# Performance work log

Hardware: AMD Instinct MI355X
Metric: run time of the kernel (lower is better)

The kernel has to match this reference:

```python
import jax, jax.numpy as jnp
import numpy as np

K = 2          # top-k experts kept (init kwarg k)
TEMP = 1.0     # gating temperature


def setup_inputs() -> dict:
    key = jax.random.key(0)
    ks = jax.random.split(key, 5)
    B, S, D, O, E = 4, 2048, 1024, 1024, 8
    scale = 1.0 / np.sqrt(D)
    x = jax.random.normal(ks[0], (B, S, D), dtype=jnp.float32)
    W = jax.random.normal(ks[1], (E, O, D), dtype=jnp.float32) * scale   # per-expert Linear weight [out,in]
    b = jax.random.normal(ks[2], (E, O), dtype=jnp.float32) * 0.01
    Wg = jax.random.normal(ks[3], (E, D), dtype=jnp.float32) * scale     # gate Linear weight [E,in]
    bg = jnp.zeros((E,), dtype=jnp.float32)
    return {"x": x, "W": W, "b": b, "Wg": Wg, "bg": bg}


def reference(x, W, b, Wg, bg):
    # gating: softmax over experts (per token, segment_expert_trigger=False)
    gate_logits = (jnp.einsum('bsd,ed->bse', x, Wg) + bg) / TEMP
    gate_scores = jax.nn.softmax(gate_logits, axis=-1)                   # [B,S,E]
    topk_scores, topk_idx = jax.lax.top_k(gate_scores, K)                # [B,S,K]
    # dense all-expert projection (matches torch.stack of per-expert Linear)
    expert_outputs = jnp.einsum('bsd,eod->bseo', x, W) + b               # [B,S,E,O]
    # gather the top-k expert outputs, scale by gate score, and sum
    selected = jnp.take_along_axis(expert_outputs, topk_idx[..., None], axis=2)  # [B,S,K,O]
    output = jnp.sum(selected * topk_scores[..., None], axis=2)          # [B,S,O]
    return output
```

## Files before the change

### kernel.cpp

```cpp
#include <hip/hip_runtime.h>
#include <hip/hip_bf16.h>

#define NTOK 8192
#define DDIM 1024
#define ODIM 1024
#define NEXP 8
#define BK   64
#define NKT  (DDIM / BK)

typedef __attribute__((ext_vector_type(8))) short short8;
typedef __attribute__((ext_vector_type(4))) float f32x4;

#define CNT_OFF   0u
#define SC_OFF    256u
#define LIST_OFF  (128u * 1024u)
#define XH_OFF    (1u<<20)
#define WH_OFF    ((1u<<20) + NTOK*DDIM*2u)

__device__ inline unsigned short f2bf(float f) {
    unsigned int u = __float_as_uint(f);
    unsigned int r = (u + 0x7FFFu + ((u >> 16) & 1u)) >> 16;
    return (unsigned short)r;
}

__device__ inline void glds16(const unsigned short* g, unsigned short* l) {
    __builtin_amdgcn_global_load_lds(
        (const __attribute__((address_space(1))) unsigned int*)g,
        (__attribute__((address_space(3))) unsigned int*)l, 16, 0, 0);
}

__global__ void k_zero(int* counts) {
    if (threadIdx.x < 16) counts[threadIdx.x] = 0;
}

__global__ void k_cvt(const float4* __restrict__ src, ushort4* __restrict__ dst, int n4) {
    int i = blockIdx.x * blockDim.x + threadIdx.x;
    if (i >= n4) return;
    float4 v = src[i];
    ushort4 o;
    o.x = f2bf(v.x); o.y = f2bf(v.y); o.z = f2bf(v.z); o.w = f2bf(v.w);
    dst[i] = o;
}

__global__ __launch_bounds__(256) void k_gate(
    const float* __restrict__ x, const float* __restrict__ Wg,
    const float* __restrict__ bg, const float* __restrict__ b,
    float* __restrict__ out, float* __restrict__ scores2,
    int* __restrict__ lists, int* __restrict__ counts,
    unsigned short* __restrict__ xh)
{
    __shared__ unsigned char s_eid[64];
    const int tid = threadIdx.x, wave = tid >> 6, lane = tid & 63;
    const int tblk = blockIdx.x * 32;

    double bgv[NEXP];
    #pragma unroll
    for (int e = 0; e < NEXP; e++) bgv[e] = (double)bg[e];

    for (int ti = 0; ti < 8; ti++) {
        const int t = tblk + wave * 8 + ti;
        const float* xr = x + (size_t)t * DDIM;
        float4 xv[4];
        #pragma unroll
        for (int i = 0; i < 4; i++)
            xv[i] = *(const float4*)&xr[lane * 4 + 256 * i];

        unsigned short* xhr = xh + (size_t)t * DDIM;
        #pragma unroll
        for (int i = 0; i < 4; i++) {
            ushort4 h;
            h.x = f2bf(xv[i].x); h.y = f2bf(xv[i].y);
            h.z = f2bf(xv[i].z); h.w = f2bf(xv[i].w);
            *(ushort4*)&xhr[lane * 4 + 256 * i] = h;
        }

        double lg[NEXP];
        #pragma unroll
        for (int e = 0; e < NEXP; e++) {
            const float* wr = Wg + (size_t)e * DDIM;
            double a = 0.0;
            #pragma unroll
            for (int i = 0; i < 4; i++) {
                float4 wv = *(const float4*)&wr[lane * 4 + 256 * i];
                a += (double)xv[i].x * (double)wv.x + (double)xv[i].y * (double)wv.y
                   + (double)xv[i].z * (double)wv.z + (double)xv[i].w * (double)wv.w;
            }
            #pragma unroll
            for (int off = 32; off > 0; off >>= 1) a += __shfl_xor(a, off);
            lg[e] = a + bgv[e];
        }

        int i0 = -1, i1 = -1;
        double best = -1e300, sec = -1e300;
        #pragma unroll
        for (int e = 0; e < NEXP; e++) {
            double v = lg[e];
            if (v > best) { sec = best; i1 = i0; best = v; i0 = e; }
            else if (v > sec) { sec = v; i1 = e; }
        }
        double sum = 0.0;
        #pragma unroll
        for (int e = 0; e < NEXP; e++) sum += exp(lg[e] - best);
        float s0 = (float)(1.0 / sum);
        float s1 = (float)(exp(sec - best) / sum);

        if (lane == 0) {
            scores2[t * 2 + 0] = s0;
            scores2[t * 2 + 1] = s1;
            int le = (wave * 8 + ti) * 2;
            s_eid[le + 0] = (unsigned char)i0;
            s_eid[le + 1] = (unsigned char)i1;
        }

        const float* b0 = b + (size_t)i0 * ODIM;
        const float* b1 = b + (size_t)i1 * ODIM;
        float* orow = out + (size_t)t * ODIM;
        #pragma unroll
        for (int i = 0; i < 4; i++) {
            int o = lane * 4 + 256 * i;
            float4 v0 = *(const float4*)&b0[o];
            float4 v1 = *(const float4*)&b1[o];
            float4 r;
            r.x = s0 * v0.x + s1 * v1.x;
            r.y = s0 * v0.y + s1 * v1.y;
            r.z = s0 * v0.z + s1 * v1.z;
            r.w = s0 * v0.w + s1 * v1.w;
            *(float4*)&orow[o] = r;
        }
    }
    __syncthreads();

    if (tid < 16) {
        int e = tid & 7, kk = tid >> 3;
        int c = 0;
        for (int j = kk; j < 64; j += 2) c += (s_eid[j] == e);
        if (c) {
            int p = atomicAdd(&counts[tid], c);
            for (int j = kk; j < 64; j += 2)
                if (s_eid[j] == e)
                    lists[tid * NTOK + (p++)] = (tblk + (j >> 1)) * 2 + kk;
        }
    }
}

__global__ __launch_bounds__(256, 2) void k_gemm(
    const unsigned short* __restrict__ xh, const unsigned short* __restrict__ wh,
    const int* __restrict__ counts, const int* __restrict__ lists,
    const float* __restrict__ scores2, float* __restrict__ out)
{
    __shared__ __align__(16) unsigned short As[2][128 * BK];
    __shared__ __align__(16) unsigned short Bs[2][128 * BK];

    const int nwg = (int)gridDim.x;
    int bid = ((int)blockIdx.x & 7) * (nwg >> 3) + ((int)blockIdx.x >> 3);

    int e = -1, mt = 0, nt = 0, cnt = 0;
    #pragma unroll
    for (int ee = 0; ee < NEXP; ee++) {
        int c = counts[ee];
        int tiles = ((c + 127) >> 7) * 8;
        if (e < 0) {
            if (bid < tiles) { e = ee; mt = bid >> 3; nt = bid & 7; cnt = c; }
            else bid -= tiles;
        }
    }
    if (e < 0) return;

    const int m0 = mt * 128, n0 = nt * 128;
    const int* list = lists + e * NTOK;
    const int tid = threadIdx.x, wid = tid >> 6, lane = tid & 63;

    const int l8 = lane >> 3, s8 = lane & 7;
    const int co = ((s8 ^ l8) << 3);
    const unsigned short* whE = wh + (size_t)e * ODIM * DDIM;
    const unsigned short* aSrc[4];
    const unsigned short* bSrc[4];
    int rbase[4];
    #pragma unroll
    for (int i = 0; i < 4; i++) {
        int rb = (wid * 4 + i) * 8;
        rbase[i] = rb;
        int r = rb + l8;
        int g = m0 + r; if (g >= cnt) g = cnt - 1;
        aSrc[i] = xh + (size_t)(list[g] >> 1) * DDIM + co;
        bSrc[i] = whE + (size_t)(n0 + r) * DDIM + co;
    }

    const int wm = wid >> 1, wn = wid & 1;
    const int fr = lane & 15, g4 = lane >> 4;
    const int fx0 = ((g4 ^ (fr & 7)) << 3);
    const int fx1 = (((4 + g4) ^ (fr & 7)) << 3);

    f32x4 acc[4][4];
    #pragma unroll
    for (int m = 0; m < 4; m++)
        #pragma unroll
        for (int n = 0; n < 4; n++)
            acc[m][n] = (f32x4){0.f, 0.f, 0.f, 0.f};

    #pragma unroll
    for (int i = 0; i < 4; i++) {
        glds16(aSrc[i], &As[0][rbase[i] * BK]);
        glds16(bSrc[i], &Bs[0][rbase[i] * BK]);
    }

    int buf = 0;
    for (int t = 0; t < NKT; t++) {
        __syncthreads();
        if (t + 1 < NKT) {
            const int k0 = (t + 1) * BK;
            #pragma unroll
            for (int i = 0; i < 4; i++) {
                glds16(aSrc[i] + k0, &As[buf ^ 1][rbase[i] * BK]);
                glds16(bSrc[i] + k0, &Bs[buf ^ 1][rbase[i] * BK]);
            }
        }
        short8 af[4][2], bfr[4][2];
        #pragma unroll
        for (int m = 0; m < 4; m++) {
            const int row = (wm * 64 + m * 16 + fr) * BK;
            af[m][0] = *(const short8*)&As[buf][row + fx0];
            af[m][1] = *(const short8*)&As[buf][row + fx1];
        }
        #pragma unroll
        for (int n = 0; n < 4; n++) {
            const int row = (wn * 64 + n * 16 + fr) * BK;
            bfr[n][0] = *(const short8*)&Bs[buf][row + fx0];
            bfr[n][1] = *(const short8*)&Bs[buf][row + fx1];
        }
        #pragma unroll
        for (int kk = 0; kk < 2; kk++)
            #pragma unroll
            for (int m = 0; m < 4; m++)
                #pragma unroll
                for (int n = 0; n < 4; n++)
                    acc[m][n] = __builtin_amdgcn_mfma_f32_16x16x32_bf16(
                        af[m][kk], bfr[n][kk], acc[m][n], 0, 0, 0);
        buf ^= 1;
    }

    #pragma unroll
    for (int m = 0; m < 4; m++) {
        #pragma unroll
        for (int j = 0; j < 4; j++) {
            int r = wm * 64 + m * 16 + g4 * 4 + j;
            int gr = m0 + r;
            if (gr < cnt) {
                int entry = list[gr];
                int tok = entry >> 1;
                float s = scores2[entry];
                float* orow = out + (size_t)tok * ODIM + n0 + wn * 64 + fr;
                #pragma unroll
                for (int n = 0; n < 4; n++)
                    orow[n * 16] += s * acc[m][n][j];
            }
        }
    }
}

extern "C" void kernel_launch(void* const* d_in, const int* in_sizes, int n_in,
                              void* d_out, int out_size, void* d_ws, size_t ws_size,
                              hipStream_t stream) {
    const float* x  = (const float*)d_in[0];
    const float* W  = (const float*)d_in[1];
    const float* b  = (const float*)d_in[2];
    const float* Wg = (const float*)d_in[3];
    const float* bg = (const float*)d_in[4];
    float* out = (float*)d_out;
    char* ws = (char*)d_ws;

    int*   counts  = (int*)(ws + CNT_OFF);
    float* scores2 = (float*)(ws + SC_OFF);
    int*   lists   = (int*)(ws + LIST_OFF);
    unsigned short* xh = (unsigned short*)(ws + XH_OFF);
    unsigned short* wh = (unsigned short*)(ws + WH_OFF);

    k_zero<<<1, 64, 0, stream>>>(counts);

    int n4w = NEXP * ODIM * DDIM / 4;
    k_cvt<<<n4w / 256, 256, 0, stream>>>((const float4*)W, (ushort4*)wh, n4w);

    k_gate<<<NTOK / 32, 256, 0, stream>>>(x, Wg, bg, b, out, scores2, lists, counts, xh);

    k_gemm<<<576, 256, 0, stream>>>(xh, wh, counts,     lists,            scores2, out);
    k_gemm<<<576, 256, 0, stream>>>(xh, wh, counts + 8, lists + 8 * NTOK, scores2, out);
}
```

Before: 167.5 us.

## Merge expert GEMMs into one persistent launch with side buffer and smaller tiles

The two per-slot GEMM launches become one persistent, grid-strided kernel that covers all 16 expert lists. Second-slot results go to a separate buffer, and a final add kernel merges it into the output. The change also halves BK to 32 with a new LDS swizzle, raises occupancy to 4 blocks per SM, shrinks the gate kernel to 8 tokens per block with float softmax, and folds the counter zeroing into the weight-convert kernel. The aim is to cut launch count, fill the machine better and avoid serialising the two GEMM passes, at the cost of an extra output-sized buffer plus a read-modify-write pass.

```diff
diff --git a/kernel.cpp b/kernel.cpp
--- a/kernel.cpp
+++ b/kernel.cpp
@@ -5,17 +5,19 @@
 #define DDIM 1024
 #define ODIM 1024
 #define NEXP 8
-#define BK   64
+#define BK   32
 #define NKT  (DDIM / BK)
 
 typedef __attribute__((ext_vector_type(8))) short short8;
 typedef __attribute__((ext_vector_type(4))) float f32x4;
 
 #define CNT_OFF   0u
-#define SC_OFF    256u
+#define SC_OFF    (4u * 1024u)
 #define LIST_OFF  (128u * 1024u)
-#define XH_OFF    (1u<<20)
-#define WH_OFF    ((1u<<20) + NTOK*DDIM*2u)
+#define XH_OFF    (1u << 20)
+#define WH_OFF    ((1u << 20) + 16u*1024u*1024u)
+#define O2_OFF    ((1u << 20) + 32u*1024u*1024u)
+#define WS_NEED   ((size_t)O2_OFF + (size_t)NTOK * ODIM * 4u)
 
 __device__ inline unsigned short f2bf(float f) {
     unsigned int u = __float_as_uint(f);
@@ -29,11 +31,9 @@
         (__attribute__((address_space(3))) unsigned int*)l, 16, 0, 0);
 }
 
-__global__ void k_zero(int* counts) {
-    if (threadIdx.x < 16) counts[threadIdx.x] = 0;
-}
-
-__global__ void k_cvt(const float4* __restrict__ src, ushort4* __restrict__ dst, int n4) {
+__global__ void k_cvtw(const float4* __restrict__ src, ushort4* __restrict__ dst,
+                       int n4, int* __restrict__ counts) {
+    if (blockIdx.x == 0 && threadIdx.x < 16) counts[threadIdx.x] = 0;
     int i = blockIdx.x * blockDim.x + threadIdx.x;
     if (i >= n4) return;
     float4 v = src[i];
@@ -42,23 +42,20 @@
     dst[i] = o;
 }
 
-__global__ __launch_bounds__(256) void k_gate(
+__global__ __launch_bounds__(256, 2) void k_gate(
     const float* __restrict__ x, const float* __restrict__ Wg,
     const float* __restrict__ bg, const float* __restrict__ b,
     float* __restrict__ out, float* __restrict__ scores2,
     int* __restrict__ lists, int* __restrict__ counts,
     unsigned short* __restrict__ xh)
 {
-    __shared__ unsigned char s_eid[64];
+    __shared__ unsigned char s_eid[16];
     const int tid = threadIdx.x, wave = tid >> 6, lane = tid & 63;
-    const int tblk = blockIdx.x * 32;
-
-    double bgv[NEXP];
-    #pragma unroll
-    for (int e = 0; e < NEXP; e++) bgv[e] = (double)bg[e];
-
-    for (int ti = 0; ti < 8; ti++) {
-        const int t = tblk + wave * 8 + ti;
+    const int tblk = blockIdx.x * 8;
+
+    #pragma unroll 1
+    for (int ti = 0; ti < 2; ti++) {
+        const int t = tblk + wave * 2 + ti;
         const float* xr = x + (size_t)t * DDIM;
         float4 xv[4];
         #pragma unroll
@@ -87,7 +84,7 @@
             }
             #pragma unroll
             for (int off = 32; off > 0; off >>= 1) a += __shfl_xor(a, off);
-            lg[e] = a + bgv[e];
+            lg[e] = a + (double)bg[e];
         }
 
         int i0 = -1, i1 = -1;
@@ -98,16 +95,16 @@
             if (v > best) { sec = best; i1 = i0; best = v; i0 = e; }
             else if (v > sec) { sec = v; i1 = e; }
         }
-        double sum = 0.0;
-        #pragma unroll
-        for (int e = 0; e < NEXP; e++) sum += exp(lg[e] - best);
-        float s0 = (float)(1.0 / sum);
-        float s1 = (float)(exp(sec - best) / sum);
+        float sum = 0.f;
+        #pragma unroll
+        for (int e = 0; e < NEXP; e++) sum += expf((float)(lg[e] - best));
+        float s0 = 1.f / sum;
+        float s1 = expf((float)(sec - best)) / sum;
 
         if (lane == 0) {
             scores2[t * 2 + 0] = s0;
             scores2[t * 2 + 1] = s1;
-            int le = (wave * 8 + ti) * 2;
+            int le = (wave * 2 + ti) * 2;
             s_eid[le + 0] = (unsigned char)i0;
             s_eid[le + 1] = (unsigned char)i1;
         }
@@ -133,128 +130,153 @@
     if (tid < 16) {
         int e = tid & 7, kk = tid >> 3;
         int c = 0;
-        for (int j = kk; j < 64; j += 2) c += (s_eid[j] == e);
+        #pragma unroll
+        for (int j = 0; j < 8; j++) c += (s_eid[j * 2 + kk] == e);
         if (c) {
             int p = atomicAdd(&counts[tid], c);
-            for (int j = kk; j < 64; j += 2)
-                if (s_eid[j] == e)
-                    lists[tid * NTOK + (p++)] = (tblk + (j >> 1)) * 2 + kk;
-        }
-    }
-}
-
-__global__ __launch_bounds__(256, 2) void k_gemm(
+            #pragma unroll
+            for (int j = 0; j < 8; j++)
+                if (s_eid[j * 2 + kk] == e)
+                    lists[tid * NTOK + (p++)] = (tblk + j) * 2 + kk;
+        }
+    }
+}
+
+__global__ __launch_bounds__(256, 4) void k_gemm(
     const unsigned short* __restrict__ xh, const unsigned short* __restrict__ wh,
     const int* __restrict__ counts, const int* __restrict__ lists,
-    const float* __restrict__ scores2, float* __restrict__ out)
+    const float* __restrict__ scores2, float* __restrict__ out,
+    float* __restrict__ out2, int listLo, int listHi)
 {
     __shared__ __align__(16) unsigned short As[2][128 * BK];
     __shared__ __align__(16) unsigned short Bs[2][128 * BK];
 
     const int nwg = (int)gridDim.x;
-    int bid = ((int)blockIdx.x & 7) * (nwg >> 3) + ((int)blockIdx.x >> 3);
-
-    int e = -1, mt = 0, nt = 0, cnt = 0;
+    const int bid0 = ((int)blockIdx.x & 7) * (nwg >> 3) + ((int)blockIdx.x >> 3);
+    const int tid = threadIdx.x, wid = tid >> 6, lane = tid & 63;
+
+    int cnts[16];
     #pragma unroll
-    for (int ee = 0; ee < NEXP; ee++) {
-        int c = counts[ee];
-        int tiles = ((c + 127) >> 7) * 8;
-        if (e < 0) {
-            if (bid < tiles) { e = ee; mt = bid >> 3; nt = bid & 7; cnt = c; }
-            else bid -= tiles;
-        }
-    }
-    if (e < 0) return;
-
-    const int m0 = mt * 128, n0 = nt * 128;
-    const int* list = lists + e * NTOK;
-    const int tid = threadIdx.x, wid = tid >> 6, lane = tid & 63;
-
-    const int l8 = lane >> 3, s8 = lane & 7;
-    const int co = ((s8 ^ l8) << 3);
-    const unsigned short* whE = wh + (size_t)e * ODIM * DDIM;
-    const unsigned short* aSrc[4];
-    const unsigned short* bSrc[4];
-    int rbase[4];
+    for (int i = 0; i < 16; i++) cnts[i] = counts[i];
+    int tbLo = 0, tbHi = 0;
     #pragma unroll
-    for (int i = 0; i < 4; i++) {
-        int rb = (wid * 4 + i) * 8;
-        rbase[i] = rb;
-        int r = rb + l8;
-        int g = m0 + r; if (g >= cnt) g = cnt - 1;
-        aSrc[i] = xh + (size_t)(list[g] >> 1) * DDIM + co;
-        bSrc[i] = whE + (size_t)(n0 + r) * DDIM + co;
-    }
-
+    for (int i = 0; i < 16; i++) {
+        int nt_ = ((cnts[i] + 127) >> 7) * 8;
+        if (i < listLo) tbLo += nt_;
+        if (i < listHi) tbHi += nt_;
+    }
+
+    const int rl = lane >> 2;
     const int wm = wid >> 1, wn = wid & 1;
     const int fr = lane & 15, g4 = lane >> 4;
-    const int fx0 = ((g4 ^ (fr & 7)) << 3);
-    const int fx1 = (((4 + g4) ^ (fr & 7)) << 3);
-
-    f32x4 acc[4][4];
-    #pragma unroll
-    for (int m = 0; m < 4; m++)
-        #pragma unroll
-        for (int n = 0; n < 4; n++)
-            acc[m][n] = (f32x4){0.f, 0.f, 0.f, 0.f};
-
-    #pragma unroll
-    for (int i = 0; i < 4; i++) {
-        glds16(aSrc[i], &As[0][rbase[i] * BK]);
-        glds16(bSrc[i], &Bs[0][rbase[i] * BK]);
-    }
-
-    int buf = 0;
-    for (int t = 0; t < NKT; t++) {
-        __syncthreads();
-        if (t + 1 < NKT) {
-            const int k0 = (t + 1) * BK;
-            #pragma unroll
-            for (int i = 0; i < 4; i++) {
-                glds16(aSrc[i] + k0, &As[buf ^ 1][rbase[i] * BK]);
-                glds16(bSrc[i] + k0, &Bs[buf ^ 1][rbase[i] * BK]);
-            }
-        }
-        short8 af[4][2], bfr[4][2];
-        #pragma unroll
-        for (int m = 0; m < 4; m++) {
-            const int row = (wm * 64 + m * 16 + fr) * BK;
-            af[m][0] = *(const short8*)&As[buf][row + fx0];
-            af[m][1] = *(const short8*)&As[buf][row + fx1];
-        }
-        #pragma unroll
-        for (int n = 0; n < 4; n++) {
-            const int row = (wn * 64 + n * 16 + fr) * BK;
-            bfr[n][0] = *(const short8*)&Bs[buf][row + fx0];
-            bfr[n][1] = *(const short8*)&Bs[buf][row + fx1];
-        }
-        #pragma unroll
-        for (int kk = 0; kk < 2; kk++)
+
+    #pragma unroll 1
+    for (int tile = tbLo + bid0; tile < tbHi; tile += nwg) {
+        int li = 0, base = 0, cnt = 0, acc_ = 0;
+        #pragma unroll
+        for (int i = 0; i < 16; i++) {
+            int nt_ = ((cnts[i] + 127) >> 7) * 8;
+            if (tile >= acc_) { li = i; base = acc_; cnt = cnts[i]; }
+            acc_ += nt_;
+        }
+        const int local = tile - base, mt = local >> 3, ntc = local & 7;
+        const int m0 = mt * 128, n0 = ntc * 128;
+        const int* list = lists + li * NTOK;
+        const unsigned short* whE = wh + (size_t)(li & 7) * ODIM * DDIM;
+        const bool st = (out2 != nullptr) && (li >= 8);
+
+        const unsigned short* aS[2];
+        const unsigned short* bS[2];
+        int rb[2];
+        #pragma unroll
+        for (int i = 0; i < 2; i++) {
+            int R = wid * 32 + i * 16 + rl;
+            int sl = (lane & 3) ^ ((R >> 1) & 3);
+            int g = m0 + R; if (g >= cnt) g = cnt - 1;
+            aS[i] = xh + (size_t)(list[g] >> 1) * DDIM + sl * 8;
+            bS[i] = whE + (size_t)(n0 + R) * DDIM + sl * 8;
+            rb[i] = (wid * 32 + i * 16) * BK;
+        }
+
+        f32x4 acc[4][4];
+        #pragma unroll
+        for (int m = 0; m < 4; m++)
+            #pragma unroll
+            for (int n = 0; n < 4; n++)
+                acc[m][n] = (f32x4){0.f, 0.f, 0.f, 0.f};
+
+        #pragma unroll
+        for (int i = 0; i < 2; i++) {
+            glds16(aS[i], &As[0][rb[i]]);
+            glds16(bS[i], &Bs[0][rb[i]]);
+        }
+
+        int buf = 0;
+        #pragma unroll 1
+        for (int t = 0; t < NKT; t++) {
+            __syncthreads();
+            if (t + 1 < NKT) {
+                const int k0 = (t + 1) * BK;
+                #pragma unroll
+                for (int i = 0; i < 2; i++) {
+                    glds16(aS[i] + k0, &As[buf ^ 1][rb[i]]);
+                    glds16(bS[i] + k0, &Bs[buf ^ 1][rb[i]]);
+                }
+            }
+            short8 af[4], bf_[4];
+            #pragma unroll
+            for (int m = 0; m < 4; m++) {
+                int R = wm * 64 + m * 16 + fr;
+                int ph = g4 ^ ((R >> 1) & 3);
+                af[m] = *(const short8*)&As[buf][R * BK + ph * 8];
+            }
+            #pragma unroll
+            for (int n = 0; n < 4; n++) {
+                int R = wn * 64 + n * 16 + fr;
+                int ph = g4 ^ ((R >> 1) & 3);
+                bf_[n] = *(const short8*)&Bs[buf][R * BK + ph * 8];
+            }
             #pragma unroll
             for (int m = 0; m < 4; m++)
                 #pragma unroll
                 for (int n = 0; n < 4; n++)
                     acc[m][n] = __builtin_amdgcn_mfma_f32_16x16x32_bf16(
-                        af[m][kk], bfr[n][kk], acc[m][n], 0, 0, 0);
-        buf ^= 1;
-    }
-
-    #pragma unroll
-    for (int m = 0; m < 4; m++) {
-        #pragma unroll
-        for (int j = 0; j < 4; j++) {
-            int r = wm * 64 + m * 16 + g4 * 4 + j;
-            int gr = m0 + r;
-            if (gr < cnt) {
-                int entry = list[gr];
-                int tok = entry >> 1;
-                float s = scores2[entry];
-                float* orow = out + (size_t)tok * ODIM + n0 + wn * 64 + fr;
-                #pragma unroll
-                for (int n = 0; n < 4; n++)
-                    orow[n * 16] += s * acc[m][n][j];
-            }
-        }
+                        af[m], bf_[n], acc[m][n], 0, 0, 0);
+            buf ^= 1;
+        }
+
+        #pragma unroll
+        for (int m = 0; m < 4; m++) {
+            #pragma unroll
+            for (int j = 0; j < 4; j++) {
+                int r = wm * 64 + m * 16 + g4 * 4 + j;
+                int gr = m0 + r;
+                if (gr < cnt) {
+                    int entry = list[gr];
+                    float s = scores2[entry];
+                    float* orow = (st ? out2 : out)
+                                  + (size_t)(entry >> 1) * ODIM + n0 + wn * 64 + fr;
+                    if (st) {
+                        #pragma unroll
+                        for (int n = 0; n < 4; n++) orow[n * 16] = s * acc[m][n][j];
+                    } else {
+                        #pragma unroll
+                        for (int n = 0; n < 4; n++) orow[n * 16] += s * acc[m][n][j];
+                    }
+                }
+            }
+        }
+    }
+}
+
+__global__ void k_add(float4* __restrict__ out, const float4* __restrict__ out2, int n4) {
+    int i = blockIdx.x * blockDim.x + threadIdx.x;
+    const int stride = gridDim.x * blockDim.x;
+    #pragma unroll 1
+    for (; i < n4; i += stride) {
+        float4 a = out[i], c = out2[i];
+        a.x += c.x; a.y += c.y; a.z += c.z; a.w += c.w;
+        out[i] = a;
     }
 }
 
@@ -274,14 +296,18 @@
     int*   lists   = (int*)(ws + LIST_OFF);
     unsigned short* xh = (unsigned short*)(ws + XH_OFF);
     unsigned short* wh = (unsigned short*)(ws + WH_OFF);
-
-    k_zero<<<1, 64, 0, stream>>>(counts);
+    float* out2 = (float*)(ws + O2_OFF);
 
     int n4w = NEXP * ODIM * DDIM / 4;
-    k_cvt<<<n4w / 256, 256, 0, stream>>>((const float4*)W, (ushort4*)wh, n4w);
-
-    k_gate<<<NTOK / 32, 256, 0, stream>>>(x, Wg, bg, b, out, scores2, lists, counts, xh);
-
-    k_gemm<<<576, 256, 0, stream>>>(xh, wh, counts,     lists,            scores2, out);
-    k_gemm<<<576, 256, 0, stream>>>(xh, wh, counts + 8, lists + 8 * NTOK, scores2, out);
-}
+    k_cvtw<<<n4w / 256, 256, 0, stream>>>((const float4*)W, (ushort4*)wh, n4w, counts);
+
+    k_gate<<<NTOK / 8, 256, 0, stream>>>(x, Wg, bg, b, out, scores2, lists, counts, xh);
+
+    if (ws_size >= WS_NEED) {
+        k_gemm<<<1024, 256, 0, stream>>>(xh, wh, counts, lists, scores2, out, out2, 0, 16);
+        k_add<<<2048, 256, 0, stream>>>((float4*)out, (const float4*)out2, NTOK * ODIM / 4);
+    } else {
+        k_gemm<<<1024, 256, 0, stream>>>(xh, wh, counts, lists, scores2, out, nullptr, 0, 8);
+        k_gemm<<<1024, 256, 0, stream>>>(xh, wh, counts, lists, scores2, out, nullptr, 8, 16);
+    }
+}
```

Result: slower. 188.5 us (+12.5%).
